# Optimization experiments

Hardware: AMD Instinct MI355X
Metric: run time of the kernel (lower is better)

The kernel has to match this reference:

```python
import jax, jax.numpy as jnp
import numpy as np

N = 50000   # nodes
E = 800000  # edges (avg degree 16)
D = 256     # node feature dim
H = 4       # heads per layer
C = 64      # per-head channels
L = 3       # depth
SCALE = 1.0 / (C ** 0.5)


def setup_inputs() -> dict:
    key = jax.random.key(0)
    ks = jax.random.split(key, 11)
    w = 0.05
    return {
        "x": jax.random.normal(ks[0], (N, D), jnp.float32),
        "edge_index": jax.random.randint(ks[1], (2, E), 0, N, dtype=jnp.int32),
        "Wq": jax.random.normal(ks[2], (L, D, H * C), jnp.float32) * w,
        "bq": jax.random.normal(ks[3], (L, H * C), jnp.float32) * w,
        "Wk": jax.random.normal(ks[4], (L, D, H * C), jnp.float32) * w,
        "bk": jax.random.normal(ks[5], (L, H * C), jnp.float32) * w,
        "Wv": jax.random.normal(ks[6], (L, D, H * C), jnp.float32) * w,
        "bv": jax.random.normal(ks[7], (L, H * C), jnp.float32) * w,
        "Ws": jax.random.normal(ks[8], (L, D, H * C), jnp.float32) * w,
        "bs": jax.random.normal(ks[9], (L, H * C), jnp.float32) * w,
    }


def _segment_softmax(alpha, seg, num_segments):
    # alpha: [E, H], seg: [E] destination node ids
    amax = jax.ops.segment_max(alpha, seg, num_segments=num_segments)  # [N, H]
    amax = jnp.where(jnp.isfinite(amax), amax, 0.0)  # isolated nodes -> -inf
    ex = jnp.exp(alpha - amax[seg])
    denom = jax.ops.segment_sum(ex, seg, num_segments=num_segments)  # [N, H]
    return ex / (denom[seg] + 1e-16)


def reference(x, edge_index, Wq, bq, Wk, bk, Wv, bv, Ws, bs):
    # PyG TransformerConv, heads=H, concat=True, root_weight=True, no edge features.
    src = edge_index[0]  # message source j
    dst = edge_index[1]  # message target i
    h = x
    for l in range(L):
        q = (h @ Wq[l] + bq[l]).reshape(N, H, C)
        k = (h @ Wk[l] + bk[l]).reshape(N, H, C)
        v = (h @ Wv[l] + bv[l]).reshape(N, H, C)
        # per-edge attention logits [E, H]
        alpha = jnp.einsum('ehc,ehc->eh', q[dst], k[src]) * SCALE
        attn = _segment_softmax(alpha, dst, N)
        # weighted message aggregation: [E, H, C] -> [N, H, C]
        msg = v[src] * attn[..., None]
        agg = jax.ops.segment_sum(msg, dst, num_segments=N).reshape(N, H * C)
        h = jax.nn.relu(agg + h @ Ws[l] + bs[l])
    return h
```

## Files before the change

### kernel.cpp

```cpp
#include <hip/hip_runtime.h>
#include <hip/hip_bf16.h>
#include <math.h>

#define N_NODES 50000
#define N_EDGES 800000
#define ATT_SCALE 0.125f

typedef __attribute__((ext_vector_type(8))) short bf16x8;
typedef __attribute__((ext_vector_type(4))) float f32x4;

__device__ __forceinline__ unsigned short f2bf(float f) {
  __hip_bfloat16 h = __float2bfloat16(f);
  unsigned short u; __builtin_memcpy(&u, &h, 2); return u;
}
__device__ __forceinline__ float bf2f(unsigned short u) {
  __hip_bfloat16 h; __builtin_memcpy(&h, &u, 2); return __bfloat162float(h);
}
__device__ __forceinline__ void gload16(const void* g, void* l) {
  __builtin_amdgcn_global_load_lds(
      (const __attribute__((address_space(1))) unsigned int*)g,
      (__attribute__((address_space(3))) unsigned int*)l, 16, 0, 0);
}

__global__ void zero_int(int* __restrict__ p, int n) {
  int i = blockIdx.x * blockDim.x + threadIdx.x;
  if (i < n) p[i] = 0;
}

__global__ void hist_kernel(const int* __restrict__ dst, int* __restrict__ counts, int e) {
  int i = blockIdx.x * blockDim.x + threadIdx.x;
  if (i < e) atomicAdd(&counts[dst[i]], 1);
}

__global__ __launch_bounds__(1024) void scan1_kernel(const int* __restrict__ counts,
                                                     int* __restrict__ offsets,
                                                     int* __restrict__ btot, int n) {
  __shared__ int wsum[16];
  const int tid = threadIdx.x;
  const int lane = tid & 63, wid = tid >> 6;
  int idx = blockIdx.x * 1024 + tid;
  int v = (idx < n) ? counts[idx] : 0;
  int s = v;
#pragma unroll
  for (int off = 1; off < 64; off <<= 1) {
    int t = __shfl_up(s, off);
    if (lane >= off) s += t;
  }
  if (lane == 63) wsum[wid] = s;
  __syncthreads();
  if (wid == 0) {
    int wsv = (lane < 16) ? wsum[lane] : 0;
#pragma unroll
    for (int off = 1; off < 16; off <<= 1) {
      int t = __shfl_up(wsv, off);
      if (lane >= off) wsv += t;
    }
    if (lane < 16) wsum[lane] = wsv;
  }
  __syncthreads();
  int wbase = (wid > 0) ? wsum[wid - 1] : 0;
  if (idx < n) offsets[idx] = wbase + s - v;
  if (tid == 0) btot[blockIdx.x] = wsum[15];
}

__global__ __launch_bounds__(64) void scan2_kernel(int* __restrict__ btot, int nb) {
  int lane = threadIdx.x;
  int v = (lane < nb) ? btot[lane] : 0;
  int s = v;
#pragma unroll
  for (int off = 1; off < 64; off <<= 1) {
    int t = __shfl_up(s, off);
    if (lane >= off) s += t;
  }
  if (lane < nb) btot[lane] = s - v;
}

__global__ void scan3_kernel(int* __restrict__ offsets, int* __restrict__ cursor,
                             const int* __restrict__ btot, int n) {
  int i = blockIdx.x * blockDim.x + threadIdx.x;
  if (i < n) {
    int o = offsets[i] + btot[i >> 10];
    offsets[i] = o;
    cursor[i] = o;
  }
}

__global__ __launch_bounds__(1024) void scan_kernel(const int* __restrict__ counts,
                                                    int* __restrict__ offsets,
                                                    int* __restrict__ cursor, int n) {
  __shared__ int wsum[16];
  const int tid = threadIdx.x;
  const int lane = tid & 63, wid = tid >> 6;
  int carry = 0;
  for (int base = 0; base < n; base += 1024) {
    int idx = base + tid;
    int v = (idx < n) ? counts[idx] : 0;
    int s = v;
#pragma unroll
    for (int off = 1; off < 64; off <<= 1) {
      int t = __shfl_up(s, off);
      if (lane >= off) s += t;
    }
    if (lane == 63) wsum[wid] = s;
    __syncthreads();
    if (wid == 0) {
      int wsv = (lane < 16) ? wsum[lane] : 0;
#pragma unroll
      for (int off = 1; off < 16; off <<= 1) {
        int t = __shfl_up(wsv, off);
        if (lane >= off) wsv += t;
      }
      if (lane < 16) wsum[lane] = wsv;
    }
    __syncthreads();
    int wbase = (wid > 0) ? wsum[wid - 1] : 0;
    if (idx < n) {
      int ex = carry + wbase + s - v;
      offsets[idx] = ex;
      cursor[idx] = ex;
    }
    int total = wsum[15];
    __syncthreads();
    carry += total;
  }
  if (tid == 0) offsets[n] = carry;
}

__global__ void fill_kernel(const int* __restrict__ src, const int* __restrict__ dst,
                            int* __restrict__ cursor, int* __restrict__ ssrc, int e) {
  int i = blockIdx.x * blockDim.x + threadIdx.x;
  if (i < e) {
    int d = dst[i];
    int slot = atomicAdd(&cursor[d], 1);
    ssrc[slot] = src[i];
  }
}

__global__ void sort_kernel(const int* __restrict__ offsets, const int* __restrict__ counts,
                            int* __restrict__ ssrc) {
  int i = blockIdx.x * blockDim.x + threadIdx.x;
  if (i >= N_NODES) return;
  int beg = offsets[i], cnt = counts[i];
  for (int a = 1; a < cnt; a++) {
    int key = ssrc[beg + a];
    int b = a - 1;
    while (b >= 0 && ssrc[beg + b] > key) {
      ssrc[beg + b + 1] = ssrc[beg + b];
      b--;
    }
    ssrc[beg + b + 1] = key;
  }
}

__global__ void convert_x_kernel(const float* __restrict__ x,
                                 unsigned short* __restrict__ Ahi,
                                 unsigned short* __restrict__ Alo) {
  int t = blockIdx.x * blockDim.x + threadIdx.x;
  int row = t >> 6, g = (t & 63) * 4;
  if (row >= N_NODES) return;
  float4 xv = *(const float4*)(x + (size_t)row * 256 + g);
  ushort4 hi, lo;
  hi.x = f2bf(xv.x); lo.x = f2bf(xv.x - bf2f(hi.x));
  hi.y = f2bf(xv.y); lo.y = f2bf(xv.y - bf2f(hi.y));
  hi.z = f2bf(xv.z); lo.z = f2bf(xv.z - bf2f(hi.z));
  hi.w = f2bf(xv.w); lo.w = f2bf(xv.w - bf2f(hi.w));
  *(ushort4*)(Ahi + (size_t)row * 256 + g) = hi;
  *(ushort4*)(Alo + (size_t)row * 256 + g) = lo;
}

__global__ void convert_w_kernel(const float* __restrict__ Wq, const float* __restrict__ Wk,
                                 const float* __restrict__ Wv, const float* __restrict__ Ws,
                                 unsigned short* __restrict__ Bexp) {
  int t = blockIdx.x * blockDim.x + threadIdx.x;
  if (t >= 3 * 256 * 1024) return;
  int n = t & 1023;
  int k = (t >> 10) & 255;
  int l = t >> 18;
  const float* W = (n < 256) ? Wq : (n < 512) ? Wk : (n < 768) ? Wv : Ws;
  float w = W[l * 65536 + k * 256 + (n & 255)];
  unsigned short hi = f2bf(w);
  unsigned short lo = f2bf(w - bf2f(hi));
  unsigned short* row = Bexp + ((size_t)l * 1024 + n) * 768;
  row[k] = hi; row[256 + k] = lo; row[512 + k] = hi;
}

__global__ __launch_bounds__(256) void bgemm_kernel(
    const unsigned short* __restrict__ Ahi,
    const unsigned short* __restrict__ Alo,
    const unsigned short* __restrict__ B,
    const float* __restrict__ bq, const float* __restrict__ bk,
    const float* __restrict__ bv, const float* __restrict__ bs,
    int layer,
    unsigned short* __restrict__ Qb,
    unsigned short* __restrict__ KVb,
    float* __restrict__ Sf) {
  __shared__ __align__(16) char lds[49152];
  char* Al  = lds;
  char* Bl1 = lds + 16384;
  char* Bl2 = lds + 32768;

  const int orig = blockIdx.x;
  const int swz = (orig & 7) * 391 + (orig >> 3);
  const int nb = swz & 7;
  const int m0 = (swz >> 3) * 128;

  const int tid = threadIdx.x;
  const int wid = tid >> 6;
  const int lane = tid & 63;
  const int l15 = lane & 15, lhi = lane >> 4;
  const int wr = wid >> 1, wc = wid & 1;

  const char* Ag_hi = (const char*)Ahi;
  const char* Ag_lo = (const char*)Alo;
  const char* Bg = (const char*)(B + ((size_t)layer * 1024 + nb * 128) * 768);

  f32x4 acc[4][4];
#pragma unroll
  for (int m = 0; m < 4; m++)
#pragma unroll
    for (int n = 0; n < 4; n++) acc[m][n] = (f32x4){0.f, 0.f, 0.f, 0.f};

  const int swzl = (l15 & 7) << 4;

  for (int kt4 = 0; kt4 < 4; kt4++) {
    const int ka2 = kt4 * 128;
#pragma unroll
    for (int i = 0; i < 4; i++) {
      int o = tid * 16 + i * 4096;
      int row = o >> 7;
      int sg = ((o >> 4) & 7) ^ (row & 7);
      gload16(Ag_hi + (size_t)(m0 + row) * 512 + ka2 + sg * 16, Al  + wid * 1024 + i * 4096);
      gload16(Bg + (size_t)row * 1536 + ka2 + sg * 16,          Bl1 + wid * 1024 + i * 4096);
      gload16(Bg + (size_t)row * 1536 + 512 + ka2 + sg * 16,    Bl2 + wid * 1024 + i * 4096);
    }
    __syncthreads();

    bf16x8 af[2][4], bfrag[2][4];
#pragma unroll
    for (int kk = 0; kk < 2; kk++)
#pragma unroll
      for (int m = 0; m < 4; m++) {
        af[kk][m]    = *(const bf16x8*)(Al  + (wr * 64 + m * 16 + l15) * 128 + ((kk * 64 + lhi * 16) ^ swzl));
        bfrag[kk][m] = *(const bf16x8*)(Bl1 + (wc * 64 + m * 16 + l15) * 128 + ((kk * 64 + lhi * 16) ^ swzl));
      }
#pragma unroll
    for (int kk = 0; kk < 2; kk++)
#pragma unroll
      for (int m = 0; m < 4; m++)
#pragma unroll
        for (int n = 0; n < 4; n++)
          acc[m][n] = __builtin_amdgcn_mfma_f32_16x16x32_bf16(af[kk][m], bfrag[kk][n], acc[m][n], 0, 0, 0);
#pragma unroll
    for (int kk = 0; kk < 2; kk++)
#pragma unroll
      for (int m = 0; m < 4; m++)
        bfrag[kk][m] = *(const bf16x8*)(Bl2 + (wc * 64 + m * 16 + l15) * 128 + ((kk * 64 + lhi * 16) ^ swzl));
#pragma unroll
    for (int kk = 0; kk < 2; kk++)
#pragma unroll
      for (int m = 0; m < 4; m++)
#pragma unroll
        for (int n = 0; n < 4; n++)
          acc[m][n] = __builtin_amdgcn_mfma_f32_16x16x32_bf16(af[kk][m], bfrag[kk][n], acc[m][n], 0, 0, 0);
    __syncthreads();
  }

  for (int kt4 = 0; kt4 < 4; kt4++) {
    const int ka2 = kt4 * 128;
#pragma unroll
    for (int i = 0; i < 4; i++) {
      int o = tid * 16 + i * 4096;
      int row = o >> 7;
      int sg = ((o >> 4) & 7) ^ (row & 7);
      gload16(Ag_lo + (size_t)(m0 + row) * 512 + ka2 + sg * 16, Al  + wid * 1024 + i * 4096);
      gload16(Bg + (size_t)row * 1536 + 1024 + ka2 + sg * 16,   Bl1 + wid * 1024 + i * 4096);
    }
    __syncthreads();

    bf16x8 af[2][4], bfrag[2][4];
#pragma unroll
    for (int kk = 0; kk < 2; kk++)
#pragma unroll
      for (int m = 0; m < 4; m++) {
        af[kk][m]    = *(const bf16x8*)(Al  + (wr * 64 + m * 16 + l15) * 128 + ((kk * 64 + lhi * 16) ^ swzl));
        bfrag[kk][m] = *(const bf16x8*)(Bl1 + (wc * 64 + m * 16 + l15) * 128 + ((kk * 64 + lhi * 16) ^ swzl));
      }
#pragma unroll
    for (int kk = 0; kk < 2; kk++)
#pragma unroll
      for (int m = 0; m < 4; m++)
#pragma unroll
        for (int n = 0; n < 4; n++)
          acc[m][n] = __builtin_amdgcn_mfma_f32_16x16x32_bf16(af[kk][m], bfrag[kk][n], acc[m][n], 0, 0, 0);
    __syncthreads();
  }

  const float* bias = ((nb < 2) ? bq : (nb < 4) ? bk : (nb < 6) ? bv : bs) + layer * 256 + (nb & 1) * 128;
  float bn[4];
#pragma unroll
  for (int n = 0; n < 4; n++) bn[n] = bias[wc * 64 + n * 16 + l15];

  const int col = (nb & 1) * 128 + wc * 64 + l15;
  if (nb < 2) {
#pragma unroll
    for (int m = 0; m < 4; m++) {
#pragma unroll
      for (int r = 0; r < 4; r++) {
        int row = m0 + wr * 64 + m * 16 + lhi * 4 + r;
        if (row < N_NODES) {
          unsigned short* orow = Qb + (size_t)row * 256 + col;
#pragma unroll
          for (int n = 0; n < 4; n++) orow[n * 16] = f2bf(acc[m][n][r] + bn[n]);
        }
      }
    }
  } else if (nb < 6) {
    const int col512 = ((nb >= 4) ? 256 : 0) + col;
#pragma unroll
    for (int m = 0; m < 4; m++) {
#pragma unroll
      for (int r = 0; r < 4; r++) {
        int row = m0 + wr * 64 + m * 16 + lhi * 4 + r;
        if (row < N_NODES) {
          unsigned short* orow = KVb + (size_t)row * 512 + col512;
#pragma unroll
          for (int n = 0; n < 4; n++) orow[n * 16] = f2bf(acc[m][n][r] + bn[n]);
        }
      }
    }
  } else {
#pragma unroll
    for (int m = 0; m < 4; m++) {
#pragma unroll
      for (int r = 0; r < 4; r++) {
        int row = m0 + wr * 64 + m * 16 + lhi * 4 + r;
        if (row < N_NODES) {
          float* orow = Sf + (size_t)row * 256 + col;
#pragma unroll
          for (int n = 0; n < 4; n++) orow[n * 16] = acc[m][n][r] + bn[n];
        }
      }
    }
  }
}

template <int MODE>
__global__ __launch_bounds__(256) void attn_kernel(
    const unsigned short* __restrict__ Qb,
    const unsigned short* __restrict__ KVb,
    const float* __restrict__ Sf,
    const int* __restrict__ offsets,
    const int* __restrict__ counts,
    const int* __restrict__ ssrc,
    float* __restrict__ hout,
    unsigned short* __restrict__ Ahi,
    unsigned short* __restrict__ Alo) {
  int wv = threadIdx.x >> 6;
  int lane = threadIdx.x & 63;
  int i = blockIdx.x * 4 + wv;
  if (i >= N_NODES) return;

  const int off = (lane >> 4) * 64 + (lane & 15) * 4;

  ushort4 qb = *(const ushort4*)(Qb + (size_t)i * 256 + off);
  float4 q = make_float4(bf2f(qb.x), bf2f(qb.y), bf2f(qb.z), bf2f(qb.w));

  float mC[4] = {-1e30f, -1e30f, -1e30f, -1e30f};
  float sC[4] = {0.f, 0.f, 0.f, 0.f};
  float4 aC[4];
#pragma unroll
  for (int u = 0; u < 4; u++) aC[u] = make_float4(0.f, 0.f, 0.f, 0.f);

  const int beg = offsets[i];
  const int cnt = counts[i];
  int e = 0;
  for (; e + 4 <= cnt; e += 4) {
    int j[4];
#pragma unroll
    for (int u = 0; u < 4; u++) j[u] = ssrc[beg + e + u];
    ushort4 kk[4], vv[4];
#pragma unroll
    for (int u = 0; u < 4; u++) {
      const unsigned short* base = KVb + (size_t)j[u] * 512;
      kk[u] = *(const ushort4*)(base + off);
      vv[u] = *(const ushort4*)(base + 256 + off);
    }
    float p[4];
#pragma unroll
    for (int u = 0; u < 4; u++)
      p[u] = q.x * bf2f(kk[u].x) + q.y * bf2f(kk[u].y) +
             q.z * bf2f(kk[u].z) + q.w * bf2f(kk[u].w);
#pragma unroll
    for (int u = 0; u < 4; u++) p[u] += __shfl_xor(p[u], 1);
#pragma unroll
    for (int u = 0; u < 4; u++) p[u] += __shfl_xor(p[u], 2);
#pragma unroll
    for (int u = 0; u < 4; u++) p[u] += __shfl_xor(p[u], 4);
#pragma unroll
    for (int u = 0; u < 4; u++) p[u] += __shfl_xor(p[u], 8);
#pragma unroll
    for (int u = 0; u < 4; u++) {
      float pv = p[u] * ATT_SCALE;
      float mn = fmaxf(mC[u], pv);
      float c = __expf(mC[u] - mn);
      float w = __expf(pv - mn);
      sC[u] = sC[u] * c + w;
      aC[u].x = aC[u].x * c + w * bf2f(vv[u].x);
      aC[u].y = aC[u].y * c + w * bf2f(vv[u].y);
      aC[u].z = aC[u].z * c + w * bf2f(vv[u].z);
      aC[u].w = aC[u].w * c + w * bf2f(vv[u].w);
      mC[u] = mn;
    }
  }
  for (; e < cnt; e++) {
    int j1 = ssrc[beg + e];
    const unsigned short* base = KVb + (size_t)j1 * 512;
    ushort4 k1 = *(const ushort4*)(base + off);
    ushort4 v1 = *(const ushort4*)(base + 256 + off);
    float p1 = q.x * bf2f(k1.x) + q.y * bf2f(k1.y) + q.z * bf2f(k1.z) + q.w * bf2f(k1.w);
    p1 += __shfl_xor(p1, 1);
    p1 += __shfl_xor(p1, 2);
    p1 += __shfl_xor(p1, 4);
    p1 += __shfl_xor(p1, 8);
    p1 *= ATT_SCALE;
    float mn = fmaxf(mC[0], p1); float c = __expf(mC[0] - mn); float w = __expf(p1 - mn);
    sC[0] = sC[0] * c + w;
    aC[0].x = aC[0].x * c + w * bf2f(v1.x);
    aC[0].y = aC[0].y * c + w * bf2f(v1.y);
    aC[0].z = aC[0].z * c + w * bf2f(v1.z);
    aC[0].w = aC[0].w * c + w * bf2f(v1.w);
    mC[0] = mn;
  }

  float mm = fmaxf(fmaxf(mC[0], mC[1]), fmaxf(mC[2], mC[3]));
  float s = 0.f;
  float4 a = make_float4(0.f, 0.f, 0.f, 0.f);
#pragma unroll
  for (int u = 0; u < 4; u++) {
    float c = __expf(mC[u] - mm);
    s += sC[u] * c;
    a.x += aC[u].x * c;
    a.y += aC[u].y * c;
    a.z += aC[u].z * c;
    a.w += aC[u].w * c;
  }

  float4 sk = *(const float4*)(Sf + (size_t)i * 256 + off);
  float inv = 1.f / (s + 1e-16f);
  float4 o = make_float4(fmaxf(a.x * inv + sk.x, 0.f),
                         fmaxf(a.y * inv + sk.y, 0.f),
                         fmaxf(a.z * inv + sk.z, 0.f),
                         fmaxf(a.w * inv + sk.w, 0.f));
  if (MODE == 0) {
    *(float4*)(hout + (size_t)i * 256 + off) = o;
  } else {
    ushort4 hi, lo;
    hi.x = f2bf(o.x); lo.x = f2bf(o.x - bf2f(hi.x));
    hi.y = f2bf(o.y); lo.y = f2bf(o.y - bf2f(hi.y));
    hi.z = f2bf(o.z); lo.z = f2bf(o.z - bf2f(hi.z));
    hi.w = f2bf(o.w); lo.w = f2bf(o.w - bf2f(hi.w));
    *(ushort4*)(Ahi + (size_t)i * 256 + off) = hi;
    *(ushort4*)(Alo + (size_t)i * 256 + off) = lo;
  }
}

#define BM 128
#define BN 128
#define BK 16
__global__ __launch_bounds__(256) void gemm_kernel(
    const float* __restrict__ X,
    const float* __restrict__ Wq, const float* __restrict__ Wk,
    const float* __restrict__ Wv, const float* __restrict__ Ws,
    const float* __restrict__ bq, const float* __restrict__ bk,
    const float* __restrict__ bv, const float* __restrict__ bs,
    int layer, float* __restrict__ out) {
  __shared__ __align__(16) float As[BK][BM + 4];
  __shared__ __align__(16) float Bs[BK][BN + 4];
  const int m0 = blockIdx.x * BM;
  const int n0 = blockIdx.y * BN;
  const int wsel = n0 >> 8;
  const float* W;
  const float* bias;
  if (wsel == 0)      { W = Wq; bias = bq; }
  else if (wsel == 1) { W = Wk; bias = bk; }
  else if (wsel == 2) { W = Wv; bias = bv; }
  else                { W = Ws; bias = bs; }
  W += (size_t)layer * 256 * 256;
  bias += (size_t)layer * 256;
  const int nc0 = n0 & 255;
  const int tid = threadIdx.x;
  const int tx = tid & 15;
  const int ty = tid >> 4;
  float acc[8][8];
#pragma unroll
  for (int i = 0; i < 8; i++)
#pragma unroll
    for (int j = 0; j < 8; j++) acc[i][j] = 0.f;
  for (int k0 = 0; k0 < 256; k0 += BK) {
#pragma unroll
    for (int i = 0; i < 8; i++) {
      int idx = tid + i * 256;
      int r = idx >> 4, c = idx & 15;
      int gr = m0 + r;
      As[c][r] = (gr < N_NODES) ? X[(size_t)gr * 256 + k0 + c] : 0.f;
    }
#pragma unroll
    for (int i = 0; i < 8; i++) {
      int idx = tid + i * 256;
      int r = idx >> 7, c = idx & 127;
      Bs[r][c] = W[(size_t)(k0 + r) * 256 + nc0 + c];
    }
    __syncthreads();
#pragma unroll
    for (int k = 0; k < BK; k++) {
      float4 a0 = *(const float4*)&As[k][ty * 8];
      float4 a1 = *(const float4*)&As[k][ty * 8 + 4];
      float4 b0 = *(const float4*)&Bs[k][tx * 8];
      float4 b1 = *(const float4*)&Bs[k][tx * 8 + 4];
      float a[8] = {a0.x, a0.y, a0.z, a0.w, a1.x, a1.y, a1.z, a1.w};
      float b[8] = {b0.x, b0.y, b0.z, b0.w, b1.x, b1.y, b1.z, b1.w};
#pragma unroll
      for (int mi = 0; mi < 8; mi++)
#pragma unroll
        for (int ni = 0; ni < 8; ni++) acc[mi][ni] = fmaf(a[mi], b[ni], acc[mi][ni]);
    }
    __syncthreads();
  }
  float bl[8];
#pragma unroll
  for (int ni = 0; ni < 8; ni++) bl[ni] = bias[nc0 + tx * 8 + ni];
#pragma unroll
  for (int mi = 0; mi < 8; mi++) {
    int row = m0 + ty * 8 + mi;
    if (row < N_NODES) {
      float* orow = out + (size_t)row * 1024 + n0 + tx * 8;
      float4 o0 = make_float4(acc[mi][0] + bl[0], acc[mi][1] + bl[1],
                              acc[mi][2] + bl[2], acc[mi][3] + bl[3]);
      float4 o1 = make_float4(acc[mi][4] + bl[4], acc[mi][5] + bl[5],
                              acc[mi][6] + bl[6], acc[mi][7] + bl[7]);
      *(float4*)orow = o0;
      *(float4*)(orow + 4) = o1;
    }
  }
}

__global__ __launch_bounds__(256) void attn_legacy(
    const float* __restrict__ qkvs,
    const int* __restrict__ offsets,
    const int* __restrict__ counts,
    const int* __restrict__ ssrc,
    float* __restrict__ hout) {
  int wv = threadIdx.x >> 6;
  int lane = threadIdx.x & 63;
  int i = blockIdx.x * 4 + wv;
  if (i >= N_NODES) return;
  const int off = (lane >> 4) * 64 + (lane & 15) * 4;
  const float* base_i = qkvs + (size_t)i * 1024;
  float4 q = *(const float4*)(base_i + off);
  float m = -INFINITY, s = 0.f;
  float4 a = make_float4(0.f, 0.f, 0.f, 0.f);
  int beg = offsets[i];
  int cnt = counts[i];
  for (int e = 0; e < cnt; e++) {
    int j = ssrc[beg + e];
    const float* base_j = qkvs + (size_t)j * 1024;
    float4 k = *(const float4*)(base_j + 256 + off);
    float p = q.x * k.x + q.y * k.y + q.z * k.z + q.w * k.w;
    p += __shfl_xor(p, 1);
    p += __shfl_xor(p, 2);
    p += __shfl_xor(p, 4);
    p += __shfl_xor(p, 8);
    p *= ATT_SCALE;
    float4 v = *(const float4*)(base_j + 512 + off);
    float mn = fmaxf(m, p);
    float c = __expf(m - mn);
    float w = __expf(p - mn);
    s = s * c + w;
    a.x = a.x * c + w * v.x;
    a.y = a.y * c + w * v.y;
    a.z = a.z * c + w * v.z;
    a.w = a.w * c + w * v.w;
    m = mn;
  }
  float4 sk = *(const float4*)(base_i + 768 + off);
  float inv = 1.f / (s + 1e-16f);
  float4 o = make_float4(fmaxf(a.x * inv + sk.x, 0.f),
                         fmaxf(a.y * inv + sk.y, 0.f),
                         fmaxf(a.z * inv + sk.z, 0.f),
                         fmaxf(a.w * inv + sk.w, 0.f));
  *(float4*)(hout + (size_t)i * 256 + off) = o;
}

extern "C" void kernel_launch(void* const* d_in, const int* in_sizes, int n_in,
                              void* d_out, int out_size, void* d_ws, size_t ws_size,
                              hipStream_t stream) {
  (void)in_sizes; (void)n_in; (void)out_size;
  const float* x   = (const float*)d_in[0];
  const int*   ei  = (const int*)d_in[1];
  const float* Wq  = (const float*)d_in[2];
  const float* bq  = (const float*)d_in[3];
  const float* Wk  = (const float*)d_in[4];
  const float* bk  = (const float*)d_in[5];
  const float* Wv  = (const float*)d_in[6];
  const float* bv  = (const float*)d_in[7];
  const float* Ws_ = (const float*)d_in[8];
  const float* bs  = (const float*)d_in[9];
  float* out = (float*)d_out;

  const int* src = ei;
  const int* dst = ei + N_EDGES;
  char* ws = (char*)d_ws;

  const size_t NEED = 187768064ull;
  bool big = ws_size >= NEED;

  if (big) {
    unsigned short* Qb   = (unsigned short*)(ws + 0);
    unsigned short* KVb  = (unsigned short*)(ws + 25600000);
    float*          Sf   = (float*)(ws + 76800000);
    unsigned short* Ahi  = (unsigned short*)(ws + 128000000);
    unsigned short* Alo  = (unsigned short*)(ws + 153624576);
    unsigned short* Bexp = (unsigned short*)(ws + 179249152);
    int* counts = (int*)(ws + 183967744);
    int* offs   = (int*)(ws + 184167744);
    int* cursor = (int*)(ws + 184367808);
    int* ssrc   = (int*)(ws + 184567808);
    int* btot   = (int*)(ws + 187767808);

    zero_int<<<(N_NODES + 255) / 256, 256, 0, stream>>>(counts, N_NODES);
    hist_kernel<<<(N_EDGES + 255) / 256, 256, 0, stream>>>(dst, counts, N_EDGES);
    scan1_kernel<<<(N_NODES + 1023) / 1024, 1024, 0, stream>>>(counts, offs, btot, N_NODES);
    scan2_kernel<<<1, 64, 0, stream>>>(btot, (N_NODES + 1023) / 1024);
    scan3_kernel<<<(N_NODES + 255) / 256, 256, 0, stream>>>(offs, cursor, btot, N_NODES);
    fill_kernel<<<(N_EDGES + 255) / 256, 256, 0, stream>>>(src, dst, cursor, ssrc, N_EDGES);
    sort_kernel<<<(N_NODES + 255) / 256, 256, 0, stream>>>(offs, counts, ssrc);

    convert_w_kernel<<<3072, 256, 0, stream>>>(Wq, Wk, Wv, Ws_, Bexp);
    convert_x_kernel<<<(N_NODES * 64 + 255) / 256, 256, 0, stream>>>(x, Ahi, Alo);

    for (int l = 0; l < 3; l++) {
      bgemm_kernel<<<3128, 256, 0, stream>>>(Ahi, Alo, Bexp, bq, bk, bv, bs, l, Qb, KVb, Sf);
      if (l < 2)
        attn_kernel<1><<<(N_NODES + 3) / 4, 256, 0, stream>>>(Qb, KVb, Sf, offs, counts, ssrc,
                                                              nullptr, Ahi, Alo);
      else
        attn_kernel<0><<<(N_NODES + 3) / 4, 256, 0, stream>>>(Qb, KVb, Sf, offs, counts, ssrc,
                                                              out, nullptr, nullptr);
    }
  } else {
    float* qkvs   = (float*)(ws + 0);
    float* hbuf   = (float*)(ws + 204800000);
    int*   counts = (int*)(ws + 256000000);
    int*   offs   = (int*)(ws + 256200064);
    int*   cursor = (int*)(ws + 256400128);
    int*   ssrc   = (int*)(ws + 256600192);

    zero_int<<<(N_NODES + 255) / 256, 256, 0, stream>>>(counts, N_NODES);
    hist_kernel<<<(N_EDGES + 255) / 256, 256, 0, stream>>>(dst, counts, N_EDGES);
    scan_kernel<<<1, 1024, 0, stream>>>(counts, offs, cursor, N_NODES);
    fill_kernel<<<(N_EDGES + 255) / 256, 256, 0, stream>>>(src, dst, cursor, ssrc, N_EDGES);

    dim3 ggrid((N_NODES + BM - 1) / BM, 1024 / BN);
    for (int l = 0; l < 3; l++) {
      const float* hin = (l == 0) ? x : hbuf;
      float* hout = (l == 2) ? out : hbuf;
      gemm_kernel<<<ggrid, 256, 0, stream>>>(hin, Wq, Wk, Wv, Ws_, bq, bk, bv, bs, l, qkvs);
      attn_legacy<<<(N_NODES + 3) / 4, 256, 0, stream>>>(qkvs, offs, counts, ssrc, hout);
    }
  }
}
```

Baseline: 896.9 us.

## Use lazy single-accumulator online softmax and drop per-node edge sort

```diff
diff --git a/kernel.cpp b/kernel.cpp
--- a/kernel.cpp
+++ b/kernel.cpp
@@ -133,22 +133,6 @@
     int d = dst[i];
     int slot = atomicAdd(&cursor[d], 1);
     ssrc[slot] = src[i];
-  }
-}
-
-__global__ void sort_kernel(const int* __restrict__ offsets, const int* __restrict__ counts,
-                            int* __restrict__ ssrc) {
-  int i = blockIdx.x * blockDim.x + threadIdx.x;
-  if (i >= N_NODES) return;
-  int beg = offsets[i], cnt = counts[i];
-  for (int a = 1; a < cnt; a++) {
-    int key = ssrc[beg + a];
-    int b = a - 1;
-    while (b >= 0 && ssrc[beg + b] > key) {
-      ssrc[beg + b + 1] = ssrc[beg + b];
-      b--;
-    }
-    ssrc[beg + b + 1] = key;
   }
 }
 
@@ -365,11 +349,8 @@
   ushort4 qb = *(const ushort4*)(Qb + (size_t)i * 256 + off);
   float4 q = make_float4(bf2f(qb.x), bf2f(qb.y), bf2f(qb.z), bf2f(qb.w));
 
-  float mC[4] = {-1e30f, -1e30f, -1e30f, -1e30f};
-  float sC[4] = {0.f, 0.f, 0.f, 0.f};
-  float4 aC[4];
-#pragma unroll
-  for (int u = 0; u < 4; u++) aC[u] = make_float4(0.f, 0.f, 0.f, 0.f);
+  float m = -1e30f, s = 0.f;
+  float4 a = make_float4(0.f, 0.f, 0.f, 0.f);
 
   const int beg = offsets[i];
   const int cnt = counts[i];
@@ -399,17 +380,23 @@
 #pragma unroll
     for (int u = 0; u < 4; u++) p[u] += __shfl_xor(p[u], 8);
 #pragma unroll
+    for (int u = 0; u < 4; u++) p[u] *= ATT_SCALE;
+
+    float bm = fmaxf(fmaxf(p[0], p[1]), fmaxf(p[2], p[3]));
+    if (!__all(bm <= m + 8.f)) {
+      float mn = fmaxf(m, bm);
+      float c = __expf(m - mn);
+      s *= c; a.x *= c; a.y *= c; a.z *= c; a.w *= c;
+      m = mn;
+    }
+#pragma unroll
     for (int u = 0; u < 4; u++) {
-      float pv = p[u] * ATT_SCALE;
-      float mn = fmaxf(mC[u], pv);
-      float c = __expf(mC[u] - mn);
-      float w = __expf(pv - mn);
-      sC[u] = sC[u] * c + w;
-      aC[u].x = aC[u].x * c + w * bf2f(vv[u].x);
-      aC[u].y = aC[u].y * c + w * bf2f(vv[u].y);
-      aC[u].z = aC[u].z * c + w * bf2f(vv[u].z);
-      aC[u].w = aC[u].w * c + w * bf2f(vv[u].w);
-      mC[u] = mn;
+      float w = __expf(p[u] - m);
+      s += w;
+      a.x += w * bf2f(vv[u].x);
+      a.y += w * bf2f(vv[u].y);
+      a.z += w * bf2f(vv[u].z);
+      a.w += w * bf2f(vv[u].w);
     }
   }
   for (; e < cnt; e++) {
@@ -423,26 +410,18 @@
     p1 += __shfl_xor(p1, 4);
     p1 += __shfl_xor(p1, 8);
     p1 *= ATT_SCALE;
-    float mn = fmaxf(mC[0], p1); float c = __expf(mC[0] - mn); float w = __expf(p1 - mn);
-    sC[0] = sC[0] * c + w;
-    aC[0].x = aC[0].x * c + w * bf2f(v1.x);
-    aC[0].y = aC[0].y * c + w * bf2f(v1.y);
-    aC[0].z = aC[0].z * c + w * bf2f(v1.z);
-    aC[0].w = aC[0].w * c + w * bf2f(v1.w);
-    mC[0] = mn;
-  }
-
-  float mm = fmaxf(fmaxf(mC[0], mC[1]), fmaxf(mC[2], mC[3]));
-  float s = 0.f;
-  float4 a = make_float4(0.f, 0.f, 0.f, 0.f);
-#pragma unroll
-  for (int u = 0; u < 4; u++) {
-    float c = __expf(mC[u] - mm);
-    s += sC[u] * c;
-    a.x += aC[u].x * c;
-    a.y += aC[u].y * c;
-    a.z += aC[u].z * c;
-    a.w += aC[u].w * c;
+    if (!__all(p1 <= m + 8.f)) {
+      float mn = fmaxf(m, p1);
+      float c = __expf(m - mn);
+      s *= c; a.x *= c; a.y *= c; a.z *= c; a.w *= c;
+      m = mn;
+    }
+    float w = __expf(p1 - m);
+    s += w;
+    a.x += w * bf2f(v1.x);
+    a.y += w * bf2f(v1.y);
+    a.z += w * bf2f(v1.z);
+    a.w += w * bf2f(v1.w);
   }
 
   float4 sk = *(const float4*)(Sf + (size_t)i * 256 + off);
@@ -633,7 +612,6 @@
     scan2_kernel<<<1, 64, 0, stream>>>(btot, (N_NODES + 1023) / 1024);
     scan3_kernel<<<(N_NODES + 255) / 256, 256, 0, stream>>>(offs, cursor, btot, N_NODES);
     fill_kernel<<<(N_EDGES + 255) / 256, 256, 0, stream>>>(src, dst, cursor, ssrc, N_EDGES);
-    sort_kernel<<<(N_NODES + 255) / 256, 256, 0, stream>>>(offs, counts, ssrc);
 
     convert_w_kernel<<<3072, 256, 0, stream>>>(Wq, Wk, Wv, Ws_, Bexp);
     convert_x_kernel<<<(N_NODES * 64 + 255) / 256, 256, 0, stream>>>(x, Ahi, Alo);
```

New measurement: 827.8 us. -7.7%, faster.
